# Performance work log

Hardware: AMD Instinct MI355X
Metric: run time of the kernel (lower is better)

The kernel has to match this reference:

```python
import jax, jax.numpy as jnp
import numpy as np
import math

H = 8
D_MODEL = 512
D_K = D_MODEL // H          # 64, per-head value dim
D_QK = D_K // 2             # 32, per-head query/key dim
B, S = 2, 4096


def setup_inputs() -> dict:
    key = jax.random.key(0)
    ks = jax.random.split(key, 20)
    std = 0.02
    inp = {
        'query': jax.random.normal(ks[0], (B, S, D_MODEL), jnp.float32),
        'key':   jax.random.normal(ks[1], (B, S, D_MODEL), jnp.float32),
        'value': jax.random.normal(ks[2], (B, S, D_MODEL), jnp.float32),
        # MLP_q: d_model -> 2*d_model -> d_model/2
        'Wq1': jax.random.normal(ks[3], (D_MODEL, 2 * D_MODEL), jnp.float32) * std,
        'bq1': jnp.zeros((2 * D_MODEL,), jnp.float32),
        'Wq2': jax.random.normal(ks[4], (2 * D_MODEL, D_MODEL // 2), jnp.float32) * std,
        'bq2': jnp.zeros((D_MODEL // 2,), jnp.float32),
        # MLP_k: d_model -> 2*d_model -> d_model/2
        'Wk1': jax.random.normal(ks[5], (D_MODEL, 2 * D_MODEL), jnp.float32) * std,
        'bk1': jnp.zeros((2 * D_MODEL,), jnp.float32),
        'Wk2': jax.random.normal(ks[6], (2 * D_MODEL, D_MODEL // 2), jnp.float32) * std,
        'bk2': jnp.zeros((D_MODEL // 2,), jnp.float32),
        # linear_v and output linear: d_model -> d_model
        'Wv': jax.random.normal(ks[7], (D_MODEL, D_MODEL), jnp.float32) * std,
        'bv': jnp.zeros((D_MODEL,), jnp.float32),
        'Wo': jax.random.normal(ks[8], (D_MODEL, D_MODEL), jnp.float32) * std,
        'bo': jnp.zeros((D_MODEL,), jnp.float32),
    }
    return inp


def reference(query, key, value, Wq1, bq1, Wq2, bq2, Wk1, bk1, Wk2, bk2, Wv, bv, Wo, bo):
    nb = query.shape[0]
    # MLP_q / MLP_k: Linear -> exact GELU -> Linear (torch GELU default is erf)
    q = jax.nn.gelu(query @ Wq1 + bq1, approximate=False) @ Wq2 + bq2   # [B,S,D_MODEL/2]
    k = jax.nn.gelu(key   @ Wk1 + bk1, approximate=False) @ Wk2 + bk2   # [B,S,D_MODEL/2]
    v = value @ Wv + bv                                                  # [B,S,D_MODEL]

    q = q.reshape(nb, -1, H, D_QK)   # [B,S,H,d_qk]
    k = k.reshape(nb, -1, H, D_QK)
    v = v.reshape(nb, -1, H, D_K)    # [B,S,H,d_k]

    # scores scaled by sqrt(d_qk) since query.size(-1) == d_k//2 in the original
    scores = jnp.einsum('bqhd,bkhd->bhqk', q, k) / math.sqrt(D_QK)  # [B,H,S,S]
    p = jax.nn.softmax(scores, axis=-1)
    x = jnp.einsum('bhqk,bkhd->bqhd', p, v).reshape(nb, -1, H * D_K)  # [B,S,D_MODEL]
    return x @ Wo + bo
```

## Files before the change

### kernel.cpp

```cpp
#include <hip/hip_runtime.h>
#include <math.h>

typedef __attribute__((ext_vector_type(8))) short short8;
typedef __bf16 bf16x8 __attribute__((ext_vector_type(8)));
typedef __attribute__((ext_vector_type(4))) float f32x4;
typedef __attribute__((ext_vector_type(16))) float f32x16;

__device__ inline short f2bf(float f) {
    unsigned u = __builtin_bit_cast(unsigned, f);
    u += 0x7fff + ((u >> 16) & 1);
    return (short)(u >> 16);
}
__device__ inline float bf2f(short h) {
    return __builtin_bit_cast(float, ((unsigned)(unsigned short)h) << 16);
}
__device__ inline float gelu_f(float x) {
    return 0.5f * x * (1.f + erff(x * 0.70710678118654752f));
}

__global__ __launch_bounds__(256) void cast3(
    const float* __restrict__ q, const float* __restrict__ k,
    const float* __restrict__ v,
    short* __restrict__ qc, short* __restrict__ kc, short* __restrict__ vc)
{
    const float* src = blockIdx.y == 0 ? q : (blockIdx.y == 1 ? k : v);
    short* dst = blockIdx.y == 0 ? qc : (blockIdx.y == 1 ? kc : vc);
    size_t i = ((size_t)blockIdx.x * 256 + threadIdx.x) * 8;
    float4 a = *(const float4*)(src + i);
    float4 b = *(const float4*)(src + i + 4);
    short8 o;
    o[0] = f2bf(a.x); o[1] = f2bf(a.y); o[2] = f2bf(a.z); o[3] = f2bf(a.w);
    o[4] = f2bf(b.x); o[5] = f2bf(b.y); o[6] = f2bf(b.z); o[7] = f2bf(b.w);
    *(short8*)(void*)(dst + i) = o;
}

__global__ __launch_bounds__(256) void wcast_t(
    const float* __restrict__ W, short* __restrict__ Wt, int K, int N)
{
    __shared__ float T[32][33];
    int k0 = blockIdx.y * 32, n0 = blockIdx.x * 32;
    int tid = threadIdx.x;
    int r = tid >> 3, c4 = (tid & 7) * 4;
    float4 v = *(const float4*)&W[(size_t)(k0 + r) * N + n0 + c4];
    T[r][c4 + 0] = v.x; T[r][c4 + 1] = v.y; T[r][c4 + 2] = v.z; T[r][c4 + 3] = v.w;
    __syncthreads();
    short4 o;
    o.x = f2bf(T[c4 + 0][r]);
    o.y = f2bf(T[c4 + 1][r]);
    o.z = f2bf(T[c4 + 2][r]);
    o.w = f2bf(T[c4 + 3][r]);
    *(short4*)&Wt[(size_t)(n0 + r) * K + k0 + c4] = o;
}

__global__ __launch_bounds__(256) void wcast_t3(
    const float* __restrict__ W, short* __restrict__ W3t, int K, int N)
{
    __shared__ float T[32][33];
    int k0 = blockIdx.y * 32, n0 = blockIdx.x * 32;
    int tid = threadIdx.x;
    int r = tid >> 3, c4 = (tid & 7) * 4;
    float4 v = *(const float4*)&W[(size_t)(k0 + r) * N + n0 + c4];
    T[r][c4 + 0] = v.x; T[r][c4 + 1] = v.y; T[r][c4 + 2] = v.z; T[r][c4 + 3] = v.w;
    __syncthreads();
    short4 hi, lo;
    float f;
    f = T[c4 + 0][r]; hi.x = f2bf(f); lo.x = f2bf(f - bf2f(hi.x));
    f = T[c4 + 1][r]; hi.y = f2bf(f); lo.y = f2bf(f - bf2f(hi.y));
    f = T[c4 + 2][r]; hi.z = f2bf(f); lo.z = f2bf(f - bf2f(hi.z));
    f = T[c4 + 3][r]; hi.w = f2bf(f); lo.w = f2bf(f - bf2f(hi.w));
    short* d = W3t + (size_t)(n0 + r) * 3 * K + k0 + c4;
    *(short4*)d = hi;
    *(short4*)(d + K) = lo;
    *(short4*)(d + 2 * K) = hi;
}

template <int ACT, int OUTF32, int BN>
__global__ __launch_bounds__(256) void gemm_bt(
    const short* __restrict__ A0, const short* __restrict__ A1,
    const short* __restrict__ B0, const short* __restrict__ B1,
    const float* __restrict__ b0, const float* __restrict__ b1,
    void* C0_, void* C1_,
    float s0, float s1, int nbn, int N, int K)
{
    constexpr int NT = BN / 32;
    const int z = blockIdx.z;
    const short* A = z ? A1 : A0;
    const short* B = z ? B1 : B0;
    const float* bias = z ? b1 : b0;
    void* C_ = z ? C1_ : C0_;
    const float scale = z ? s1 : s0;

    const int L = blockIdx.x;
    const int xcd = L & 7;
    const int per = L >> 3;
    const int bn = (per % nbn) * BN;
    const int bm = ((per / nbn) * 8 + xcd) * 128;

    const int tid = threadIdx.x;
    const int w = tid >> 6;
    const int lane = tid & 63;
    const int l15 = lane & 15, quad = lane >> 4;
    const int wm = (w >> 1) * 64, wn = (w & 1) * (BN / 2);

    __shared__ __align__(16) short As[128 * 64];
    __shared__ __align__(16) short Bs[BN * 64];

    f32x4 acc[4][NT];
#pragma unroll
    for (int mt = 0; mt < 4; ++mt)
#pragma unroll
        for (int nt = 0; nt < NT; ++nt) acc[mt][nt] = (f32x4){0.f, 0.f, 0.f, 0.f};

    for (int k0 = 0; k0 < K; k0 += 64) {
#pragma unroll
        for (int i = 0; i < 4; ++i) {
            int ga = tid + i * 256;
            int row = ga >> 3, g = ga & 7;
            short8 aval = *(const short8*)(const void*)&A[(size_t)(bm + row) * K + k0 + g * 8];
            *(short8*)(void*)&As[row * 64 + ((g ^ (row & 7)) * 8)] = aval;
        }
#pragma unroll
        for (int i = 0; i < BN / 32; ++i) {
            int gb = tid + i * 256;
            int row = gb >> 3, g = gb & 7;
            short8 bval = *(const short8*)(const void*)&B[(size_t)(bn + row) * K + k0 + g * 8];
            *(short8*)(void*)&Bs[row * 64 + ((g ^ (row & 7)) * 8)] = bval;
        }
        __syncthreads();

#pragma unroll
        for (int ks = 0; ks < 2; ++ks) {
            bf16x8 af[4], bfr[NT];
#pragma unroll
            for (int t = 0; t < 4; ++t) {
                int row = wm + t * 16 + l15;
                af[t] = __builtin_bit_cast(bf16x8,
                    *(const short8*)(const void*)&As[row * 64 + (((ks * 4 + quad) ^ (row & 7)) * 8)]);
            }
#pragma unroll
            for (int t = 0; t < NT; ++t) {
                int row = wn + t * 16 + l15;
                bfr[t] = __builtin_bit_cast(bf16x8,
                    *(const short8*)(const void*)&Bs[row * 64 + (((ks * 4 + quad) ^ (row & 7)) * 8)]);
            }
#pragma unroll
            for (int mt = 0; mt < 4; ++mt)
#pragma unroll
                for (int nt = 0; nt < NT; ++nt)
                    acc[mt][nt] = __builtin_amdgcn_mfma_f32_16x16x32_bf16(af[mt], bfr[nt], acc[mt][nt], 0, 0, 0);
        }
        __syncthreads();
    }

    float bv[NT];
#pragma unroll
    for (int nt = 0; nt < NT; ++nt) bv[nt] = bias[bn + wn + nt * 16 + l15];
#pragma unroll
    for (int mt = 0; mt < 4; ++mt)
#pragma unroll
        for (int r = 0; r < 4; ++r) {
            int row = bm + wm + mt * 16 + quad * 4 + r;
#pragma unroll
            for (int nt = 0; nt < NT; ++nt) {
                float v = acc[mt][nt][r] + bv[nt];
                if (ACT) v = gelu_f(v);
                v *= scale;
                int col = bn + wn + nt * 16 + l15;
                if (OUTF32) ((float*)C_)[(size_t)row * N + col] = v;
                else        ((short*)C_)[(size_t)row * N + col] = f2bf(v);
            }
        }
}

__global__ __launch_bounds__(256) void repack_k(
    const short* __restrict__ kb, short* __restrict__ kfr)
{
    const int kt = blockIdx.x, bh = blockIdx.y;
    const int b = bh >> 3, h = bh & 7;
    const int t = threadIdx.x;
    const int c = t >> 6, l = t & 63;
    const int nt = c >> 1, ks = c & 1;
    int key = kt * 64 + nt * 32 + (l & 31);
    int k = ks * 16 + (l >> 5) * 8;
    short8 v = *(const short8*)(const void*)&kb[(size_t)(b * 4096 + key) * 256 + h * 32 + k];
    *(short8*)(void*)&kfr[((((size_t)bh * 64 + kt) * 4 + c) * 64 + l) * 8] = v;
}

__global__ __launch_bounds__(256) void repack_v(
    const short* __restrict__ vbb, short* __restrict__ vfr)
{
    const int kt = blockIdx.x, bh = blockIdx.y;
    const int b = bh >> 3, h = bh & 7;
    const int t = threadIdx.x;
    __shared__ short Vt[64][72];

#pragma unroll
    for (int it = 0; it < 2; ++it) {
        int idx = t + it * 256;
        int keyr = idx >> 3, c8 = (idx & 7) * 8;
        *(short8*)(void*)&Vt[keyr][c8] =
            *(const short8*)(const void*)&vbb[(size_t)(b * 4096 + kt * 64 + keyr) * 512 + h * 64 + c8];
    }
    __syncthreads();
#pragma unroll
    for (int it = 0; it < 2; ++it) {
        int chunk = (t >> 6) * 2 + it;
        int l = t & 63;
        int dt = chunk >> 2, ks = chunk & 3;
        short8 o;
#pragma unroll
        for (int j = 0; j < 8; ++j)
            o[j] = Vt[ks * 16 + (l >> 5) * 8 + j][dt * 32 + (l & 31)];
        *(short8*)(void*)&vfr[((((size_t)bh * 64 + kt) * 8 + chunk) * 64 + l) * 8] = o;
    }
}

__global__ __launch_bounds__(128, 2) void flash_ks(
    const short* __restrict__ qb, const short* __restrict__ kfr,
    const short* __restrict__ vfr, short* __restrict__ xb3)
{
    const int L = blockIdx.x;
    const int xcd = L & 7;
    const int idx = L >> 3;
    const int bh = xcd * 2 + (idx & 1);
    const int qt = idx >> 1;
    const int b = bh >> 3, h = bh & 7;
    const int wv = threadIdx.x >> 6;
    const int lane = threadIdx.x & 63;
    const int l31 = lane & 31;
    const int half = lane >> 5;

    __shared__ __align__(16) short Pbuf[2][2][32 * 68];
    __shared__ __align__(16) float redO[64][66];
    __shared__ float redl[2][64];

    bf16x8 qf[2][2];
#pragma unroll
    for (int g = 0; g < 2; ++g) {
        const short* qrow = qb + (size_t)(b * 4096 + qt * 64 + g * 32 + l31) * 256 + h * 32 + half * 8;
        qf[g][0] = __builtin_bit_cast(bf16x8, *(const short8*)(const void*)qrow);
        qf[g][1] = __builtin_bit_cast(bf16x8, *(const short8*)(const void*)(qrow + 16));
    }

    f32x16 O[2][2];
#pragma unroll
    for (int g = 0; g < 2; ++g)
#pragma unroll
        for (int dt = 0; dt < 2; ++dt) O[g][dt] = (f32x16){};
    float la[2] = {0.f, 0.f};

    const short* kbase = kfr + ((size_t)bh * 64) * 4 * 512 + lane * 8;
    const short* vbase = vfr + ((size_t)bh * 64) * 8 * 512 + lane * 8;

    bf16x8 kc[4], kn[4];
    {
        const short* kp = kbase + (size_t)(wv * 32) * 4 * 512;
#pragma unroll
        for (int c = 0; c < 4; ++c)
            kc[c] = __builtin_bit_cast(bf16x8, *(const short8*)(const void*)(kp + c * 512));
    }

#pragma unroll 1
    for (int t = 0; t < 32; ++t) {
        const int kt = wv * 32 + t;
        bf16x8 vc[8];
        const short* vp = vbase + (size_t)kt * 8 * 512;
#pragma unroll
        for (int c = 0; c < 8; ++c)
            vc[c] = __builtin_bit_cast(bf16x8, *(const short8*)(const void*)(vp + c * 512));

        f32x16 zero{};
        f32x16 s00 = __builtin_amdgcn_mfma_f32_32x32x16_bf16(kc[0], qf[0][0], zero, 0, 0, 0);
        s00 = __builtin_amdgcn_mfma_f32_32x32x16_bf16(kc[1], qf[0][1], s00, 0, 0, 0);
        f32x16 s01 = __builtin_amdgcn_mfma_f32_32x32x16_bf16(kc[2], qf[0][0], zero, 0, 0, 0);
        s01 = __builtin_amdgcn_mfma_f32_32x32x16_bf16(kc[3], qf[0][1], s01, 0, 0, 0);
        f32x16 s10 = __builtin_amdgcn_mfma_f32_32x32x16_bf16(kc[0], qf[1][0], zero, 0, 0, 0);
        s10 = __builtin_amdgcn_mfma_f32_32x32x16_bf16(kc[1], qf[1][1], s10, 0, 0, 0);
        f32x16 s11 = __builtin_amdgcn_mfma_f32_32x32x16_bf16(kc[2], qf[1][0], zero, 0, 0, 0);
        s11 = __builtin_amdgcn_mfma_f32_32x32x16_bf16(kc[3], qf[1][1], s11, 0, 0, 0);

        if (t < 31) {
            const short* kp = kbase + (size_t)(kt + 1) * 4 * 512;
#pragma unroll
            for (int c = 0; c < 4; ++c)
                kn[c] = __builtin_bit_cast(bf16x8, *(const short8*)(const void*)(kp + c * 512));
        }

#pragma unroll
        for (int g = 0; g < 2; ++g) {
            short* Pw = &Pbuf[wv][g][0];
#pragma unroll
            for (int nt = 0; nt < 2; ++nt) {
                const f32x16& s = g ? (nt ? s11 : s10) : (nt ? s01 : s00);
#pragma unroll
                for (int r2 = 0; r2 < 4; ++r2) {
                    short4 pk;
                    float p0 = __builtin_amdgcn_exp2f(s[r2 * 4 + 0]);
                    float p1 = __builtin_amdgcn_exp2f(s[r2 * 4 + 1]);
                    float p2 = __builtin_amdgcn_exp2f(s[r2 * 4 + 2]);
                    float p3 = __builtin_amdgcn_exp2f(s[r2 * 4 + 3]);
                    la[g] += (p0 + p1) + (p2 + p3);
                    pk.x = f2bf(p0); pk.y = f2bf(p1); pk.z = f2bf(p2); pk.w = f2bf(p3);
                    *(short4*)(void*)&Pw[l31 * 68 + nt * 32 + r2 * 8 + half * 4] = pk;
                }
            }
        }

#pragma unroll
        for (int g = 0; g < 2; ++g) {
            const short* Pw = &Pbuf[wv][g][0];
            bf16x8 pf[4];
#pragma unroll
            for (int ks = 0; ks < 4; ++ks)
                pf[ks] = __builtin_bit_cast(bf16x8,
                    *(const short8*)(const void*)&Pw[l31 * 68 + ks * 16 + half * 8]);
#pragma unroll
            for (int ks = 0; ks < 4; ++ks) {
                O[g][0] = __builtin_amdgcn_mfma_f32_32x32x16_bf16(pf[ks], vc[ks], O[g][0], 0, 0, 0);
                O[g][1] = __builtin_amdgcn_mfma_f32_32x32x16_bf16(pf[ks], vc[4 + ks], O[g][1], 0, 0, 0);
            }
        }

#pragma unroll
        for (int c = 0; c < 4; ++c) kc[c] = kn[c];
    }

#pragma unroll
    for (int g = 0; g < 2; ++g) la[g] += __shfl_xor(la[g], 32);

    if (half == 0) {
        redl[wv][0 * 32 + l31] = la[0];
        redl[wv][1 * 32 + l31] = la[1];
    }
    if (wv == 1) {
#pragma unroll
        for (int g = 0; g < 2; ++g)
#pragma unroll
            for (int r = 0; r < 16; ++r) {
                int q = g * 32 + (r & 3) + 8 * (r >> 2) + 4 * half;
                redO[q][l31] = O[g][0][r];
                redO[q][32 + l31] = O[g][1][r];
            }
    }
    __syncthreads();
    if (wv == 0) {
#pragma unroll
        for (int g = 0; g < 2; ++g)
#pragma unroll
            for (int r = 0; r < 16; ++r) {
                int q = g * 32 + (r & 3) + 8 * (r >> 2) + 4 * half;
                float o0 = O[g][0][r] + redO[q][l31];
                float o1 = O[g][1][r] + redO[q][32 + l31];
                float inv = 1.f / (redl[0][q] + redl[1][q]);
                float x0 = o0 * inv, x1 = o1 * inv;
                short hi0 = f2bf(x0), hi1 = f2bf(x1);
                short lo0 = f2bf(x0 - bf2f(hi0)), lo1 = f2bf(x1 - bf2f(hi1));
                size_t row = (size_t)(b * 4096 + qt * 64 + q);
                short* d = xb3 + row * 1536 + h * 64 + l31;
                d[0] = hi0;    d[32] = hi1;
                d[512] = hi0;  d[544] = hi1;
                d[1024] = lo0; d[1056] = lo1;
            }
    }
}

extern "C" void kernel_launch(void* const* d_in, const int* in_sizes, int n_in,
                              void* d_out, int out_size, void* d_ws, size_t ws_size,
                              hipStream_t stream)
{
    const float* query = (const float*)d_in[0];
    const float* key   = (const float*)d_in[1];
    const float* value = (const float*)d_in[2];
    const float* Wq1   = (const float*)d_in[3];
    const float* bq1   = (const float*)d_in[4];
    const float* Wq2   = (const float*)d_in[5];
    const float* bq2   = (const float*)d_in[6];
    const float* Wk1   = (const float*)d_in[7];
    const float* bk1   = (const float*)d_in[8];
    const float* Wk2   = (const float*)d_in[9];
    const float* bk2   = (const float*)d_in[10];
    const float* Wv    = (const float*)d_in[11];
    const float* bv    = (const float*)d_in[12];
    const float* Wo    = (const float*)d_in[13];
    const float* bo    = (const float*)d_in[14];
    float* out = (float*)d_out;

    char* ws = (char*)d_ws;
    short* H1q   = (short*)(ws + 0);
    short* H1k   = (short*)(ws + 16777216);
    short* xb3   = (short*)(ws + 0);
    short* qcast = (short*)(ws + 33554432);
    short* kcast = (short*)(ws + 41943040);
    short* vcast = (short*)(ws + 50331648);
    short* qbb   = (short*)(ws + 33554432);
    short* kbb   = (short*)(ws + 37748736);
    short* vbb   = (short*)(ws + 41943040);
    short* kfr   = (short*)(ws + 50331648);
    short* vfr   = (short*)(ws + 54525952);
    short* Wq1t  = (short*)(ws + 62914560);
    short* Wk1t  = (short*)(ws + 63963136);
    short* Wq2t  = (short*)(ws + 65011712);
    short* Wk2t  = (short*)(ws + 65536000);
    short* Wvt   = (short*)(ws + 66060288);
    short* Wo3t  = (short*)(ws + 66584576);

    dim3 blk(256);
    const float qscale = 0.17677669529663687f * 1.4426950408889634f;

    cast3<<<dim3(2048, 3), blk, 0, stream>>>(query, key, value, qcast, kcast, vcast);
    wcast_t<<<dim3(32, 16), blk, 0, stream>>>(Wq1, Wq1t, 512, 1024);
    wcast_t<<<dim3(32, 16), blk, 0, stream>>>(Wk1, Wk1t, 512, 1024);
    wcast_t<<<dim3(8, 32), blk, 0, stream>>>(Wq2, Wq2t, 1024, 256);
    wcast_t<<<dim3(8, 32), blk, 0, stream>>>(Wk2, Wk2t, 1024, 256);
    wcast_t<<<dim3(16, 16), blk, 0, stream>>>(Wv, Wvt, 512, 512);
    wcast_t3<<<dim3(16, 16), blk, 0, stream>>>(Wo, Wo3t, 512, 512);

    gemm_bt<1, 0, 128><<<dim3(8 * 64, 1, 2), blk, 0, stream>>>(
        qcast, kcast, Wq1t, Wk1t, bq1, bk1, H1q, H1k, 1.f, 1.f, 8, 1024, 512);
    gemm_bt<0, 0, 64><<<dim3(4 * 64, 1, 2), blk, 0, stream>>>(
        H1q, H1k, Wq2t, Wk2t, bq2, bk2, qbb, kbb, qscale, 1.f, 4, 256, 1024);
    gemm_bt<0, 0, 64><<<dim3(8 * 64, 1, 1), blk, 0, stream>>>(
        vcast, vcast, Wvt, Wvt, bv, bv, vbb, vbb, 1.f, 1.f, 8, 512, 512);
    repack_k<<<dim3(64, 16), blk, 0, stream>>>(kbb, kfr);
    repack_v<<<dim3(64, 16), blk, 0, stream>>>(vbb, vfr);
    flash_ks<<<dim3(1024), dim3(128), 0, stream>>>(qbb, kfr, vfr, xb3);
    gemm_bt<0, 1, 64><<<dim3(8 * 64, 1, 1), blk, 0, stream>>>(
        xb3, xb3, Wo3t, Wo3t, bo, bo, out, out, 1.f, 1.f, 8, 512, 1536);
}
```

Baseline: 308.8 us.

## Split flash attention key range across four waves per block

The attention kernel now runs 256 threads per block, so four waves each process 16 key tiles instead of two waves each processing 32. Partial outputs and row sums are combined through a tree reduction in a shared-memory union buffer. The aim is more waves in flight per query tile, for better latency hiding and shorter per-block serial work. In exchange it adds reduction passes, extra barriers, and a higher launch-bounds occupancy target that may constrain registers.

```diff
diff --git a/kernel.cpp b/kernel.cpp
--- a/kernel.cpp
+++ b/kernel.cpp
@@ -215,7 +215,7 @@
     }
 }
 
-__global__ __launch_bounds__(128, 2) void flash_ks(
+__global__ __launch_bounds__(256, 4) void flash_ks(
     const short* __restrict__ qb, const short* __restrict__ kfr,
     const short* __restrict__ vfr, short* __restrict__ xb3)
 {
@@ -225,14 +225,12 @@
     const int bh = xcd * 2 + (idx & 1);
     const int qt = idx >> 1;
     const int b = bh >> 3, h = bh & 7;
-    const int wv = threadIdx.x >> 6;
+    const int w = threadIdx.x >> 6;
     const int lane = threadIdx.x & 63;
     const int l31 = lane & 31;
     const int half = lane >> 5;
 
-    __shared__ __align__(16) short Pbuf[2][2][32 * 68];
-    __shared__ __align__(16) float redO[64][66];
-    __shared__ float redl[2][64];
+    __shared__ __align__(16) char smem[34816];
 
     bf16x8 qf[2][2];
 #pragma unroll
@@ -254,15 +252,15 @@
 
     bf16x8 kc[4], kn[4];
     {
-        const short* kp = kbase + (size_t)(wv * 32) * 4 * 512;
+        const short* kp = kbase + (size_t)(w * 16) * 4 * 512;
 #pragma unroll
         for (int c = 0; c < 4; ++c)
             kc[c] = __builtin_bit_cast(bf16x8, *(const short8*)(const void*)(kp + c * 512));
     }
 
 #pragma unroll 1
-    for (int t = 0; t < 32; ++t) {
-        const int kt = wv * 32 + t;
+    for (int t = 0; t < 16; ++t) {
+        const int kt = w * 16 + t;
         bf16x8 vc[8];
         const short* vp = vbase + (size_t)kt * 8 * 512;
 #pragma unroll
@@ -279,7 +277,7 @@
         f32x16 s11 = __builtin_amdgcn_mfma_f32_32x32x16_bf16(kc[2], qf[1][0], zero, 0, 0, 0);
         s11 = __builtin_amdgcn_mfma_f32_32x32x16_bf16(kc[3], qf[1][1], s11, 0, 0, 0);
 
-        if (t < 31) {
+        if (t < 15) {
             const short* kp = kbase + (size_t)(kt + 1) * 4 * 512;
 #pragma unroll
             for (int c = 0; c < 4; ++c)
@@ -288,7 +286,7 @@
 
 #pragma unroll
         for (int g = 0; g < 2; ++g) {
-            short* Pw = &Pbuf[wv][g][0];
+            short* Pw = (short*)smem + (w * 2 + g) * 2176;
 #pragma unroll
             for (int nt = 0; nt < 2; ++nt) {
                 const f32x16& s = g ? (nt ? s11 : s10) : (nt ? s01 : s00);
@@ -308,7 +306,7 @@
 
 #pragma unroll
         for (int g = 0; g < 2; ++g) {
-            const short* Pw = &Pbuf[wv][g][0];
+            const short* Pw = (const short*)smem + (w * 2 + g) * 2176;
             bf16x8 pf[4];
 #pragma unroll
             for (int ks = 0; ks < 4; ++ks)
@@ -325,33 +323,60 @@
         for (int c = 0; c < 4; ++c) kc[c] = kn[c];
     }
 
-#pragma unroll
-    for (int g = 0; g < 2; ++g) la[g] += __shfl_xor(la[g], 32);
-
+    la[0] += __shfl_xor(la[0], 32);
+    la[1] += __shfl_xor(la[1], 32);
+
+    __syncthreads();
+    float* Bo0 = (float*)smem;
+    float* Bo1 = Bo0 + 64 * 66;
+    float* Bl  = Bo1 + 64 * 66;
     if (half == 0) {
-        redl[wv][0 * 32 + l31] = la[0];
-        redl[wv][1 * 32 + l31] = la[1];
-    }
-    if (wv == 1) {
+        Bl[w * 64 + l31] = la[0];
+        Bl[w * 64 + 32 + l31] = la[1];
+    }
+    if (w == 1 || w == 3) {
+        float* Bo = (w == 1) ? Bo0 : Bo1;
 #pragma unroll
         for (int g = 0; g < 2; ++g)
 #pragma unroll
             for (int r = 0; r < 16; ++r) {
                 int q = g * 32 + (r & 3) + 8 * (r >> 2) + 4 * half;
-                redO[q][l31] = O[g][0][r];
-                redO[q][32 + l31] = O[g][1][r];
-            }
-    }
-    __syncthreads();
-    if (wv == 0) {
+                Bo[q * 66 + l31] = O[g][0][r];
+                Bo[q * 66 + 32 + l31] = O[g][1][r];
+            }
+    }
+    __syncthreads();
+    if (w == 0 || w == 2) {
+        float* Bo = (w == 0) ? Bo0 : Bo1;
 #pragma unroll
         for (int g = 0; g < 2; ++g)
 #pragma unroll
             for (int r = 0; r < 16; ++r) {
                 int q = g * 32 + (r & 3) + 8 * (r >> 2) + 4 * half;
-                float o0 = O[g][0][r] + redO[q][l31];
-                float o1 = O[g][1][r] + redO[q][32 + l31];
-                float inv = 1.f / (redl[0][q] + redl[1][q]);
+                O[g][0][r] += Bo[q * 66 + l31];
+                O[g][1][r] += Bo[q * 66 + 32 + l31];
+            }
+    }
+    if (w == 2) {
+#pragma unroll
+        for (int g = 0; g < 2; ++g)
+#pragma unroll
+            for (int r = 0; r < 16; ++r) {
+                int q = g * 32 + (r & 3) + 8 * (r >> 2) + 4 * half;
+                Bo1[q * 66 + l31] = O[g][0][r];
+                Bo1[q * 66 + 32 + l31] = O[g][1][r];
+            }
+    }
+    __syncthreads();
+    if (w == 0) {
+#pragma unroll
+        for (int g = 0; g < 2; ++g)
+#pragma unroll
+            for (int r = 0; r < 16; ++r) {
+                int q = g * 32 + (r & 3) + 8 * (r >> 2) + 4 * half;
+                float o0 = O[g][0][r] + Bo1[q * 66 + l31];
+                float o1 = O[g][1][r] + Bo1[q * 66 + 32 + l31];
+                float inv = 1.f / (Bl[q] + Bl[64 + q] + Bl[128 + q] + Bl[192 + q]);
                 float x0 = o0 * inv, x1 = o1 * inv;
                 short hi0 = f2bf(x0), hi1 = f2bf(x1);
                 short lo0 = f2bf(x0 - bf2f(hi0)), lo1 = f2bf(x1 - bf2f(hi1));
@@ -423,7 +448,7 @@
         vcast, vcast, Wvt, Wvt, bv, bv, vbb, vbb, 1.f, 1.f, 8, 512, 512);
     repack_k<<<dim3(64, 16), blk, 0, stream>>>(kbb, kfr);
     repack_v<<<dim3(64, 16), blk, 0, stream>>>(vbb, vfr);
-    flash_ks<<<dim3(1024), dim3(128), 0, stream>>>(qbb, kfr, vfr, xb3);
+    flash_ks<<<dim3(1024), dim3(256), 0, stream>>>(qbb, kfr, vfr, xb3);
     gemm_bt<0, 1, 64><<<dim3(8 * 64, 1, 1), blk, 0, stream>>>(
         xb3, xb3, Wo3t, Wo3t, bo, bo, out, out, 1.f, 1.f, 8, 512, 1536);
 }
```

Result: slower. 781.8 us (+153.2%).
